# Kernel tuning notes

Measured on AMD Instinct MI355X. Metric: run time of the kernel, lower is better.

The kernel has to match this reference:

```python
import jax, jax.numpy as jnp
import numpy as np

N_ROIS = 2048
N_CLS = 21            # includes background (class 0)
N_GT = 50
IMG_H, IMG_W = 800.0, 1333.0
SCORE_T = 0.3         # thresh in forward
NMS_T = 0.3           # cfg.TEST.NMS
DEDUP_T = 0.3         # compute_iou iou_thresh
BBOX_STDS = jnp.array([0.1, 0.1, 0.2, 0.2], dtype=jnp.float32)
BBOX_MEANS = jnp.array([0.0, 0.0, 0.0, 0.0], dtype=jnp.float32)


def _rand_boxes(key, n, max_w, max_h):
    k1, k2, k3, k4 = jax.random.split(key, 4)
    x1 = jax.random.uniform(k1, (n,)) * (max_w - 64.0)
    y1 = jax.random.uniform(k2, (n,)) * (max_h - 64.0)
    bw = 16.0 + jax.random.uniform(k3, (n,)) * 240.0
    bh = 16.0 + jax.random.uniform(k4, (n,)) * 240.0
    x2 = jnp.minimum(x1 + bw, max_w - 1.0)
    y2 = jnp.minimum(y1 + bh, max_h - 1.0)
    return jnp.stack([x1, y1, x2, y2], axis=1)


def setup_inputs() -> dict:
    key = jax.random.key(0)
    k1, k2, k3, k4, k5 = jax.random.split(key, 5)
    boxes = _rand_boxes(k1, N_ROIS, IMG_W, IMG_H)
    rois_org = jnp.concatenate([jnp.zeros((N_ROIS, 1)), boxes], axis=1)[None]  # [1,N,5]
    cls_prob_org = jax.nn.softmax(2.0 * jax.random.normal(k2, (N_ROIS, N_CLS)), axis=1)[None]
    bbox_pred_org = 0.2 * jax.random.normal(k3, (N_ROIS, 4 * N_CLS))[None]
    im_info = jnp.array([[IMG_H, IMG_W, 1.0]], dtype=jnp.float32)
    gt_xyxy = _rand_boxes(k4, N_GT, IMG_W, IMG_H)
    gt_lbl = jax.random.randint(k5, (N_GT, 1), 1, N_CLS).astype(jnp.float32)
    gt_boxes = jnp.concatenate([gt_xyxy, gt_lbl], axis=1)[None]  # [1,G,5]
    return {"rois_org": rois_org, "cls_prob_org": cls_prob_org,
            "bbox_pred_org": bbox_pred_org, "im_info": im_info,
            "gt_boxes": gt_boxes, "num_boxes": N_GT}


def iou_matrix(b1, b2):
    # b1 [M,4], b2 [K,4] -> [M,K]
    a1 = (b1[:, 2] - b1[:, 0]) * (b1[:, 3] - b1[:, 1])
    a2 = (b2[:, 2] - b2[:, 0]) * (b2[:, 3] - b2[:, 1])
    lt = jnp.maximum(b1[:, None, :2], b2[None, :, :2])
    rb = jnp.minimum(b1[:, None, 2:], b2[None, :, 2:])
    wh = jnp.clip(rb - lt, 0.0)
    inter = wh[..., 0] * wh[..., 1]
    return inter / (a1[:, None] + a2[None, :] - inter + 1e-6)


def _decode_clip(boxes, deltas, im_info):
    # bbox_transform_inv + clip_boxes. boxes [N,4], deltas [N,C,4]
    w = boxes[:, 2] - boxes[:, 0] + 1.0
    h = boxes[:, 3] - boxes[:, 1] + 1.0
    cx = boxes[:, 0] + 0.5 * w
    cy = boxes[:, 1] + 0.5 * h
    d = deltas * BBOX_STDS + BBOX_MEANS  # unnormalize
    pcx = d[..., 0] * w[:, None] + cx[:, None]
    pcy = d[..., 1] * h[:, None] + cy[:, None]
    pw = jnp.exp(d[..., 2]) * w[:, None]
    ph = jnp.exp(d[..., 3]) * h[:, None]
    x1 = jnp.clip(pcx - 0.5 * pw, 0.0, im_info[0, 1] - 1.0)
    y1 = jnp.clip(pcy - 0.5 * ph, 0.0, im_info[0, 0] - 1.0)
    x2 = jnp.clip(pcx + 0.5 * pw, 0.0, im_info[0, 1] - 1.0)
    y2 = jnp.clip(pcy + 0.5 * ph, 0.0, im_info[0, 0] - 1.0)
    return jnp.stack([x1, y1, x2, y2], axis=-1)  # [N,C,4]


def _detect(rois_org, cls_prob_org, bbox_pred_org, im_info, gt_boxes, num_boxes):
    scores = cls_prob_org[0]                       # [N,C]
    boxes = rois_org[0, :, 1:5]                    # [N,4]
    n = scores.shape[0]
    deltas = bbox_pred_org[0].reshape(n, -1, 4)    # [N,C,4]
    pred = _decode_clip(boxes, deltas, im_info)    # [N,C,4]
    gt = gt_boxes[0, :num_boxes, :4]               # [G,4], static slice
    idx = jnp.arange(n)

    def per_class(cls_scores, cls_boxes):
        valid = cls_scores > SCORE_T
        order = jnp.argsort(jnp.where(valid, -cls_scores, jnp.inf))
        b = cls_boxes[order]
        v = valid[order]
        s = cls_scores[order]
        iou = iou_matrix(b, b)                     # [N,N]
        def body(i, keep):
            sup = keep[i] & (iou[i] > NMS_T) & (idx > i)
            return keep & ~sup
        keep = jax.lax.fori_loop(0, n, body, v)
        dup = jnp.any(iou_matrix(b, gt) > DEDUP_T, axis=1)  # gt dedup loop, vectorized
        m = (keep & ~dup).astype(b.dtype)
        return jnp.concatenate([b, s[:, None]], axis=1) * m[:, None]

    # classes 1..C-1; output [C-1, N, 5] with suppressed rows zeroed
    return jax.vmap(per_class, in_axes=(1, 1))(scores[:, 1:], pred[:, 1:, :])


def reference(rois_org, cls_prob_org, bbox_pred_org, im_info, gt_boxes, num_boxes):
    return _detect(rois_org, cls_prob_org, bbox_pred_org, im_info, gt_boxes, num_boxes)
```

## Files before the change

### kernel.cpp

```cpp
#include <hip/hip_runtime.h>

typedef unsigned long long u64;

#define N_ROIS 2048
#define N_CLSX 21
#define N_CLS_OUT 20
#define SCORE_T 0.3f
#define NMS_T 0.3f
#define DEDUP_T 0.3f
#define NT 256
#define NWAVES (NT / 64)
#define CPW (N_ROIS / 64 / NWAVES)
#define NFAST 128

__device__ __forceinline__ float iou_f(float ax1, float ay1, float ax2, float ay2,
                                       float aarea,
                                       float bx1, float by1, float bx2, float by2,
                                       float barea) {
    float ix1 = fmaxf(ax1, bx1), iy1 = fmaxf(ay1, by1);
    float ix2 = fminf(ax2, bx2), iy2 = fminf(ay2, by2);
    float iw = fmaxf(ix2 - ix1, 0.0f), ih = fmaxf(iy2 - iy1, 0.0f);
    float inter = iw * ih;
    return inter / (aarea + barea - inter + 1e-6f);
}

__global__ __launch_bounds__(NT) void detect_kernel(
    const float* __restrict__ rois,
    const float* __restrict__ cls_prob,
    const float* __restrict__ bbox_pred,
    const float* __restrict__ im_info,
    const float* __restrict__ gt_boxes,
    const int*   __restrict__ num_boxes,
    float* __restrict__ out)
{
    __shared__ float  vsc[N_ROIS];
    __shared__ int    vidx[N_ROIS];
    __shared__ float4 sbox[N_ROIS];
    __shared__ float  ssc[N_ROIS];
    __shared__ unsigned char keepb[N_ROIS];
    __shared__ float4 sgt[64];
    __shared__ int    wbase[NWAVES];
    __shared__ u64    kwords[2];
    __shared__ u64    dupw[2];

    const int tid = threadIdx.x;
    const int wid = tid >> 6, lane = tid & 63;
    const int cls = blockIdx.x + 1;
    const int ng = *num_boxes;
    const float W = im_info[1], H = im_info[0];
    float* o = out + (size_t)blockIdx.x * N_ROIS * 5;

    u64 masks[CPW];
    float vals[CPW];
    int mycnt = 0;
    #pragma unroll
    for (int c = 0; c < CPW; ++c) {
        int i = ((wid * CPW + c) << 6) + lane;
        float sc = cls_prob[i * N_CLSX + cls];
        vals[c] = sc;
        masks[c] = __ballot(sc > SCORE_T);
        mycnt += __popcll(masks[c]);
    }
    if (lane == 0) wbase[wid] = mycnt;
    __syncthreads();
    int base = 0;
    for (int w = 0; w < wid; ++w) base += wbase[w];
    int nvtot = 0;
    for (int w = 0; w < NWAVES; ++w) nvtot += wbase[w];
    const int nv = nvtot;
    #pragma unroll
    for (int c = 0; c < CPW; ++c) {
        int i = ((wid * CPW + c) << 6) + lane;
        u64 m = masks[c];
        if ((m >> lane) & 1ULL) {
            int pre = __popcll(m & ((1ULL << lane) - 1ULL));
            vidx[base + pre] = i;
            vsc[base + pre]  = vals[c];
        }
        base += __popcll(m);
    }
    __syncthreads();

    if (nv <= NFAST) {
        if (wid == 0) {
            float s0 = (lane < nv)      ? vsc[lane]      : 0.0f;
            float s1 = (64 + lane < nv) ? vsc[64 + lane] : 0.0f;
            int  idx0 = (lane < nv)      ? vidx[lane]      : 0;
            int  idx1 = (64 + lane < nv) ? vidx[64 + lane] : 0;

            float ax1 = rois[idx0 * 5 + 1], ay1 = rois[idx0 * 5 + 2];
            float ax2 = rois[idx0 * 5 + 3], ay2 = rois[idx0 * 5 + 4];
            const float* dpa = &bbox_pred[idx0 * 84 + cls * 4];
            float da0 = dpa[0], da1 = dpa[1], da2 = dpa[2], da3 = dpa[3];
            float bx1v = rois[idx1 * 5 + 1], by1v = rois[idx1 * 5 + 2];
            float bx2v = rois[idx1 * 5 + 3], by2v = rois[idx1 * 5 + 4];
            const float* dpb = &bbox_pred[idx1 * 84 + cls * 4];
            float db0 = dpb[0], db1 = dpb[1], db2 = dpb[2], db3 = dpb[3];

            int r0 = 0, r1 = 0;
            const int n0 = nv < 64 ? nv : 64;
            for (int u = 0; u < n0; ++u) {
                float su0 = __shfl(s0, u);
                float su1 = __shfl(s1, u);
                r0 += (su0 > s0) || (su0 == s0 && u < lane);
                r1 += (su0 > s1) || (su0 == s1);
                if (64 + u < nv) {
                    r0 += (su1 > s0);
                    r1 += (su1 > s1) || (su1 == s1 && u < lane);
                }
            }

            #define DECODE2(X1,Y1,X2,Y2,D0,D1,D2,D3,B)                       \
            {                                                                \
                float w = (X2) - (X1) + 1.0f, h = (Y2) - (Y1) + 1.0f;        \
                float cx = (X1) + 0.5f * w, cy = (Y1) + 0.5f * h;            \
                float pcx = (D0) * 0.1f * w + cx, pcy = (D1) * 0.1f * h + cy;\
                float pw = expf((D2) * 0.2f) * w, ph = expf((D3) * 0.2f) * h;\
                B.x = fminf(fmaxf(pcx - 0.5f * pw, 0.0f), W - 1.0f);         \
                B.y = fminf(fmaxf(pcy - 0.5f * ph, 0.0f), H - 1.0f);         \
                B.z = fminf(fmaxf(pcx + 0.5f * pw, 0.0f), W - 1.0f);         \
                B.w = fminf(fmaxf(pcy + 0.5f * ph, 0.0f), H - 1.0f);         \
            }
            float4 c0, c1;
            DECODE2(ax1, ay1, ax2, ay2, da0, da1, da2, da3, c0)
            DECODE2(bx1v, by1v, bx2v, by2v, db0, db1, db2, db3, c1)

            if (lane < nv)      { sbox[r0] = c0; ssc[r0] = s0; }
            if (64 + lane < nv) { sbox[r1] = c1; ssc[r1] = s1; }
        } else {
            if (wid == 3)
                for (int g = lane; g < ng; g += 64)
                    sgt[g] = make_float4(gt_boxes[g * 5 + 0], gt_boxes[g * 5 + 1],
                                         gt_boxes[g * 5 + 2], gt_boxes[g * 5 + 3]);
            float4* o4 = (float4*)o;
            float4 z4 = make_float4(0.f, 0.f, 0.f, 0.f);
            for (int t = (wid - 1) * 64 + lane; t < N_ROIS * 5 / 4; t += 192)
                o4[t] = z4;
        }
        __syncthreads();

        if (wid == 0) {
            float4 b0 = (lane < nv)      ? sbox[lane]      : make_float4(0,0,0,0);
            float4 b1 = (64 + lane < nv) ? sbox[64 + lane] : make_float4(0,0,0,0);
            float ar0 = (b0.z - b0.x) * (b0.w - b0.y);
            float ar1 = (b1.z - b1.x) * (b1.w - b1.y);
            u64 S0lo = 0, S0hi = 0, S1lo = 0, S1hi = 0;
            for (int i = 0; i < nv; ++i) {
                bool hi = i >= 64;
                int src = i & 63;
                float cx1 = __shfl(hi ? b1.x : b0.x, src);
                float cy1 = __shfl(hi ? b1.y : b0.y, src);
                float cx2 = __shfl(hi ? b1.z : b0.z, src);
                float cy2 = __shfl(hi ? b1.w : b0.w, src);
                float car = __shfl(hi ? ar1 : ar0, src);
                float i0 = iou_f(cx1, cy1, cx2, cy2, car, b0.x, b0.y, b0.z, b0.w, ar0);
                float i1 = iou_f(cx1, cy1, cx2, cy2, car, b1.x, b1.y, b1.z, b1.w, ar1);
                bool sup0 = (i0 > NMS_T) && (i < lane);
                bool sup1 = (i1 > NMS_T) && (i < 64 + lane);
                if (i < 64) {
                    S0lo |= sup0 ? (1ULL << i) : 0ULL;
                    S1lo |= sup1 ? (1ULL << i) : 0ULL;
                } else {
                    S0hi |= sup0 ? (1ULL << (i - 64)) : 0ULL;
                    S1hi |= sup1 ? (1ULL << (i - 64)) : 0ULL;
                }
            }
            bool init0 = lane < nv, init1 = 64 + lane < nv;
            u64 kw0 = __ballot(init0), kw1 = __ballot(init1);
            for (int it = 0; it < NFAST; ++it) {
                bool a0 = init0 && !((S0lo & kw0) | (S0hi & kw1));
                bool a1 = init1 && !((S1lo & kw0) | (S1hi & kw1));
                u64 nk0 = __ballot(a0), nk1 = __ballot(a1);
                bool done = (nk0 == kw0) && (nk1 == kw1);
                kw0 = nk0; kw1 = nk1;
                if (done) break;
            }
            if (lane == 0) { kwords[0] = kw0; kwords[1] = kw1; }
        } else if (wid == 1 || wid == 2) {
            int e = (wid - 1) * 64 + lane;
            bool dup = false;
            if (e < nv) {
                float4 a = sbox[e];
                float aarea = (a.z - a.x) * (a.w - a.y);
                for (int g = 0; g < ng; ++g) {
                    float4 gb = sgt[g];
                    float garea = (gb.z - gb.x) * (gb.w - gb.y);
                    dup |= iou_f(a.x, a.y, a.z, a.w, aarea,
                                 gb.x, gb.y, gb.z, gb.w, garea) > DEDUP_T;
                }
            }
            u64 wd = __ballot(dup);
            if (lane == 0) dupw[wid - 1] = wd;
        }
        __syncthreads();

        if (tid < NFAST && tid < nv) {
            bool kept = ((kwords[tid >> 6] >> (tid & 63)) & 1ULL) &&
                        !((dupw[tid >> 6] >> (tid & 63)) & 1ULL);
            if (kept) {
                float4 b = sbox[tid];
                float s = ssc[tid];
                float* orow = o + tid * 5;
                orow[0] = b.x; orow[1] = b.y; orow[2] = b.z; orow[3] = b.w;
                orow[4] = s;
            }
        }
        return;
    }

    for (int g = tid; g < ng; g += NT)
        sgt[g] = make_float4(gt_boxes[g * 5 + 0], gt_boxes[g * 5 + 1],
                             gt_boxes[g * 5 + 2], gt_boxes[g * 5 + 3]);

    for (int v = tid; v < nv; v += NT) {
        int idx = vidx[v];
        float x1 = rois[idx * 5 + 1], y1 = rois[idx * 5 + 2];
        float x2 = rois[idx * 5 + 3], y2 = rois[idx * 5 + 4];
        const float* dp = &bbox_pred[idx * 84 + cls * 4];
        float d0 = dp[0], d1 = dp[1], d2 = dp[2], d3 = dp[3];
        float sc = vsc[v];
        int r = 0;
        for (int u = 0; u < nv; ++u) {
            float su = vsc[u];
            r += (su > sc) || (su == sc && u < v);
        }
        float w = x2 - x1 + 1.0f, h = y2 - y1 + 1.0f;
        float cx = x1 + 0.5f * w, cy = y1 + 0.5f * h;
        float pcx = d0 * 0.1f * w + cx, pcy = d1 * 0.1f * h + cy;
        float pw = expf(d2 * 0.2f) * w, ph = expf(d3 * 0.2f) * h;
        float4 b;
        b.x = fminf(fmaxf(pcx - 0.5f * pw, 0.0f), W - 1.0f);
        b.y = fminf(fmaxf(pcy - 0.5f * ph, 0.0f), H - 1.0f);
        b.z = fminf(fmaxf(pcx + 0.5f * pw, 0.0f), W - 1.0f);
        b.w = fminf(fmaxf(pcy + 0.5f * ph, 0.0f), H - 1.0f);
        sbox[r] = b;
        ssc[r]  = sc;
        keepb[r] = 1;
    }
    __syncthreads();

    for (int i = 0; i < nv; ++i) {
        __syncthreads();
        if (keepb[i]) {
            float4 a = sbox[i];
            float aarea = (a.z - a.x) * (a.w - a.y);
            for (int j = i + 1 + tid; j < nv; j += NT) {
                if (keepb[j]) {
                    float4 bb = sbox[j];
                    float barea = (bb.z - bb.x) * (bb.w - bb.y);
                    if (iou_f(a.x, a.y, a.z, a.w, aarea,
                              bb.x, bb.y, bb.z, bb.w, barea) > NMS_T)
                        keepb[j] = 0;
                }
            }
        }
    }
    __syncthreads();
    for (int v = tid; v < nv; v += NT) {
        if (keepb[v]) {
            float4 a = sbox[v];
            float aarea = (a.z - a.x) * (a.w - a.y);
            bool dup = false;
            for (int g = 0; g < ng; ++g) {
                float4 gb = sgt[g];
                float garea = (gb.z - gb.x) * (gb.w - gb.y);
                dup |= iou_f(a.x, a.y, a.z, a.w, aarea,
                             gb.x, gb.y, gb.z, gb.w, garea) > DEDUP_T;
            }
            if (dup) keepb[v] = 0;
        }
    }
    __syncthreads();
    for (int t = tid; t < N_ROIS * 5; t += NT) {
        int j = t / 5, comp = t - 5 * j;
        float val = 0.0f;
        if (j < nv && keepb[j]) {
            float4 b = sbox[j];
            val = comp == 0 ? b.x : comp == 1 ? b.y : comp == 2 ? b.z :
                  comp == 3 ? b.w : ssc[j];
        }
        o[t] = val;
    }
}

extern "C" void kernel_launch(void* const* d_in, const int* in_sizes, int n_in,
                              void* d_out, int out_size, void* d_ws, size_t ws_size,
                              hipStream_t stream) {
    const float* rois      = (const float*)d_in[0];
    const float* cls_prob  = (const float*)d_in[1];
    const float* bbox_pred = (const float*)d_in[2];
    const float* im_info   = (const float*)d_in[3];
    const float* gt        = (const float*)d_in[4];
    const int*   nb        = (const int*)d_in[5];
    float* out = (float*)d_out;

    detect_kernel<<<dim3(N_CLS_OUT), dim3(NT), 0, stream>>>(
        rois, cls_prob, bbox_pred, im_info, gt, nb, out);
}
```

Before: 32.50 us.

## Remove sort barrier in fast NMS path by using score-order predicates in place

The small-candidate path no longer sorts boxes into shared memory before NMS. Wave 0 decodes boxes and builds suppression masks directly in compaction order, using a score comparison to decide priority. Wave 1-2 re-decode boxes for the GT dedup, and wave 3 computes ranks only for output placement. This removes one block barrier and a shared-memory round trip, at the cost of redundant decoding and more work in the inner loop.

Measured after the change: 30.97 us. 1.05x faster.

```diff
diff --git a/kernel.cpp b/kernel.cpp
--- a/kernel.cpp
+++ b/kernel.cpp
@@ -22,6 +22,22 @@
     float iw = fmaxf(ix2 - ix1, 0.0f), ih = fmaxf(iy2 - iy1, 0.0f);
     float inter = iw * ih;
     return inter / (aarea + barea - inter + 1e-6f);
+}
+
+#define DECODE_IDX(IDX, B)                                                    \
+{                                                                             \
+    float x1 = rois[(IDX) * 5 + 1], y1 = rois[(IDX) * 5 + 2];                 \
+    float x2 = rois[(IDX) * 5 + 3], y2 = rois[(IDX) * 5 + 4];                 \
+    const float* dp = &bbox_pred[(IDX) * 84 + cls * 4];                       \
+    float d0 = dp[0], d1 = dp[1], d2 = dp[2], d3 = dp[3];                     \
+    float w = x2 - x1 + 1.0f, h = y2 - y1 + 1.0f;                             \
+    float cx = x1 + 0.5f * w, cy = y1 + 0.5f * h;                             \
+    float pcx = d0 * 0.1f * w + cx, pcy = d1 * 0.1f * h + cy;                 \
+    float pw = expf(d2 * 0.2f) * w, ph = expf(d3 * 0.2f) * h;                 \
+    B.x = fminf(fmaxf(pcx - 0.5f * pw, 0.0f), W - 1.0f);                      \
+    B.y = fminf(fmaxf(pcy - 0.5f * ph, 0.0f), H - 1.0f);                      \
+    B.z = fminf(fmaxf(pcx + 0.5f * pw, 0.0f), W - 1.0f);                      \
+    B.w = fminf(fmaxf(pcy + 0.5f * ph, 0.0f), H - 1.0f);                      \
 }
 
 __global__ __launch_bounds__(NT) void detect_kernel(
@@ -40,7 +56,7 @@
     __shared__ unsigned char keepb[N_ROIS];
     __shared__ float4 sgt[64];
     __shared__ int    wbase[NWAVES];
-    __shared__ u64    kwords[2];
+    __shared__ int    rrank[NFAST];
     __shared__ u64    dupw[2];
 
     const int tid = threadIdx.x;
@@ -79,69 +95,24 @@
         }
         base += __popcll(m);
     }
+    if (wid == 3)
+        for (int g = lane; g < ng; g += 64)
+            sgt[g] = make_float4(gt_boxes[g * 5 + 0], gt_boxes[g * 5 + 1],
+                                 gt_boxes[g * 5 + 2], gt_boxes[g * 5 + 3]);
     __syncthreads();
 
     if (nv <= NFAST) {
+        float4 b0 = make_float4(0,0,0,0), b1 = make_float4(0,0,0,0);
+        float s0 = 0.0f, s1 = 0.0f;
+        u64 kw0 = 0, kw1 = 0;
+
         if (wid == 0) {
-            float s0 = (lane < nv)      ? vsc[lane]      : 0.0f;
-            float s1 = (64 + lane < nv) ? vsc[64 + lane] : 0.0f;
-            int  idx0 = (lane < nv)      ? vidx[lane]      : 0;
-            int  idx1 = (64 + lane < nv) ? vidx[64 + lane] : 0;
-
-            float ax1 = rois[idx0 * 5 + 1], ay1 = rois[idx0 * 5 + 2];
-            float ax2 = rois[idx0 * 5 + 3], ay2 = rois[idx0 * 5 + 4];
-            const float* dpa = &bbox_pred[idx0 * 84 + cls * 4];
-            float da0 = dpa[0], da1 = dpa[1], da2 = dpa[2], da3 = dpa[3];
-            float bx1v = rois[idx1 * 5 + 1], by1v = rois[idx1 * 5 + 2];
-            float bx2v = rois[idx1 * 5 + 3], by2v = rois[idx1 * 5 + 4];
-            const float* dpb = &bbox_pred[idx1 * 84 + cls * 4];
-            float db0 = dpb[0], db1 = dpb[1], db2 = dpb[2], db3 = dpb[3];
-
-            int r0 = 0, r1 = 0;
-            const int n0 = nv < 64 ? nv : 64;
-            for (int u = 0; u < n0; ++u) {
-                float su0 = __shfl(s0, u);
-                float su1 = __shfl(s1, u);
-                r0 += (su0 > s0) || (su0 == s0 && u < lane);
-                r1 += (su0 > s1) || (su0 == s1);
-                if (64 + u < nv) {
-                    r0 += (su1 > s0);
-                    r1 += (su1 > s1) || (su1 == s1 && u < lane);
-                }
-            }
-
-            #define DECODE2(X1,Y1,X2,Y2,D0,D1,D2,D3,B)                       \
-            {                                                                \
-                float w = (X2) - (X1) + 1.0f, h = (Y2) - (Y1) + 1.0f;        \
-                float cx = (X1) + 0.5f * w, cy = (Y1) + 0.5f * h;            \
-                float pcx = (D0) * 0.1f * w + cx, pcy = (D1) * 0.1f * h + cy;\
-                float pw = expf((D2) * 0.2f) * w, ph = expf((D3) * 0.2f) * h;\
-                B.x = fminf(fmaxf(pcx - 0.5f * pw, 0.0f), W - 1.0f);         \
-                B.y = fminf(fmaxf(pcy - 0.5f * ph, 0.0f), H - 1.0f);         \
-                B.z = fminf(fmaxf(pcx + 0.5f * pw, 0.0f), W - 1.0f);         \
-                B.w = fminf(fmaxf(pcy + 0.5f * ph, 0.0f), H - 1.0f);         \
-            }
-            float4 c0, c1;
-            DECODE2(ax1, ay1, ax2, ay2, da0, da1, da2, da3, c0)
-            DECODE2(bx1v, by1v, bx2v, by2v, db0, db1, db2, db3, c1)
-
-            if (lane < nv)      { sbox[r0] = c0; ssc[r0] = s0; }
-            if (64 + lane < nv) { sbox[r1] = c1; ssc[r1] = s1; }
-        } else {
-            if (wid == 3)
-                for (int g = lane; g < ng; g += 64)
-                    sgt[g] = make_float4(gt_boxes[g * 5 + 0], gt_boxes[g * 5 + 1],
-                                         gt_boxes[g * 5 + 2], gt_boxes[g * 5 + 3]);
-            float4* o4 = (float4*)o;
-            float4 z4 = make_float4(0.f, 0.f, 0.f, 0.f);
-            for (int t = (wid - 1) * 64 + lane; t < N_ROIS * 5 / 4; t += 192)
-                o4[t] = z4;
-        }
-        __syncthreads();
-
-        if (wid == 0) {
-            float4 b0 = (lane < nv)      ? sbox[lane]      : make_float4(0,0,0,0);
-            float4 b1 = (64 + lane < nv) ? sbox[64 + lane] : make_float4(0,0,0,0);
+            s0 = (lane < nv)      ? vsc[lane]      : 0.0f;
+            s1 = (64 + lane < nv) ? vsc[64 + lane] : 0.0f;
+            int idx0 = (lane < nv)      ? vidx[lane]      : 0;
+            int idx1 = (64 + lane < nv) ? vidx[64 + lane] : 0;
+            DECODE_IDX(idx0, b0)
+            DECODE_IDX(idx1, b1)
             float ar0 = (b0.z - b0.x) * (b0.w - b0.y);
             float ar1 = (b1.z - b1.x) * (b1.w - b1.y);
             u64 S0lo = 0, S0hi = 0, S1lo = 0, S1hi = 0;
@@ -152,11 +123,14 @@
                 float cy1 = __shfl(hi ? b1.y : b0.y, src);
                 float cx2 = __shfl(hi ? b1.z : b0.z, src);
                 float cy2 = __shfl(hi ? b1.w : b0.w, src);
-                float car = __shfl(hi ? ar1 : ar0, src);
+                float cs  = __shfl(hi ? s1   : s0,   src);
+                float car = (cx2 - cx1) * (cy2 - cy1);
                 float i0 = iou_f(cx1, cy1, cx2, cy2, car, b0.x, b0.y, b0.z, b0.w, ar0);
                 float i1 = iou_f(cx1, cy1, cx2, cy2, car, b1.x, b1.y, b1.z, b1.w, ar1);
-                bool sup0 = (i0 > NMS_T) && (i < lane);
-                bool sup1 = (i1 > NMS_T) && (i < 64 + lane);
+                bool hp0 = (cs > s0) || (cs == s0 && i < lane);
+                bool hp1 = (cs > s1) || (cs == s1 && i < 64 + lane);
+                bool sup0 = (i0 > NMS_T) && hp0;
+                bool sup1 = (i1 > NMS_T) && hp1;
                 if (i < 64) {
                     S0lo |= sup0 ? (1ULL << i) : 0ULL;
                     S1lo |= sup1 ? (1ULL << i) : 0ULL;
@@ -166,7 +140,7 @@
                 }
             }
             bool init0 = lane < nv, init1 = 64 + lane < nv;
-            u64 kw0 = __ballot(init0), kw1 = __ballot(init1);
+            kw0 = __ballot(init0); kw1 = __ballot(init1);
             for (int it = 0; it < NFAST; ++it) {
                 bool a0 = init0 && !((S0lo & kw0) | (S0hi & kw1));
                 bool a1 = init1 && !((S1lo & kw0) | (S1hi & kw1));
@@ -175,12 +149,14 @@
                 kw0 = nk0; kw1 = nk1;
                 if (done) break;
             }
-            if (lane == 0) { kwords[0] = kw0; kwords[1] = kw1; }
         } else if (wid == 1 || wid == 2) {
             int e = (wid - 1) * 64 + lane;
+            bool has = e < nv;
+            int idx = has ? vidx[e] : 0;
+            float4 a;
+            DECODE_IDX(idx, a)
             bool dup = false;
-            if (e < nv) {
-                float4 a = sbox[e];
+            if (has) {
                 float aarea = (a.z - a.x) * (a.w - a.y);
                 for (int g = 0; g < ng; ++g) {
                     float4 gb = sgt[g];
@@ -191,48 +167,60 @@
             }
             u64 wd = __ballot(dup);
             if (lane == 0) dupw[wid - 1] = wd;
+        } else {
+            float t0 = (lane < nv)      ? vsc[lane]      : 0.0f;
+            float t1 = (64 + lane < nv) ? vsc[64 + lane] : 0.0f;
+            int r0 = 0, r1 = 0;
+            const int n0 = nv < 64 ? nv : 64;
+            for (int u = 0; u < n0; ++u) {
+                float su0 = __shfl(t0, u);
+                float su1 = __shfl(t1, u);
+                r0 += (su0 > t0) || (su0 == t0 && u < lane);
+                r1 += (su0 > t1) || (su0 == t1);
+                if (64 + u < nv) {
+                    r0 += (su1 > t0);
+                    r1 += (su1 > t1) || (su1 == t1 && u < lane);
+                }
+            }
+            if (lane < nv)      rrank[lane]      = r0;
+            if (64 + lane < nv) rrank[64 + lane] = r1;
+            if (nv <= 64 && lane == 0) dupw[1] = 0ULL;
+        }
+
+        if (wid != 0) {
+            float4* o4 = (float4*)o;
+            float4 z4 = make_float4(0.f, 0.f, 0.f, 0.f);
+            for (int t = (wid - 1) * 64 + lane; t < N_ROIS * 5 / 4; t += 192)
+                o4[t] = z4;
         }
         __syncthreads();
 
-        if (tid < NFAST && tid < nv) {
-            bool kept = ((kwords[tid >> 6] >> (tid & 63)) & 1ULL) &&
-                        !((dupw[tid >> 6] >> (tid & 63)) & 1ULL);
-            if (kept) {
-                float4 b = sbox[tid];
-                float s = ssc[tid];
-                float* orow = o + tid * 5;
-                orow[0] = b.x; orow[1] = b.y; orow[2] = b.z; orow[3] = b.w;
-                orow[4] = s;
+        if (wid == 0) {
+            u64 d0 = dupw[0], d1 = dupw[1];
+            if (lane < nv && ((kw0 >> lane) & 1ULL) && !((d0 >> lane) & 1ULL)) {
+                float* orow = o + rrank[lane] * 5;
+                orow[0] = b0.x; orow[1] = b0.y; orow[2] = b0.z; orow[3] = b0.w;
+                orow[4] = s0;
+            }
+            if (64 + lane < nv && ((kw1 >> lane) & 1ULL) && !((d1 >> lane) & 1ULL)) {
+                float* orow = o + rrank[64 + lane] * 5;
+                orow[0] = b1.x; orow[1] = b1.y; orow[2] = b1.z; orow[3] = b1.w;
+                orow[4] = s1;
             }
         }
         return;
     }
-
-    for (int g = tid; g < ng; g += NT)
-        sgt[g] = make_float4(gt_boxes[g * 5 + 0], gt_boxes[g * 5 + 1],
-                             gt_boxes[g * 5 + 2], gt_boxes[g * 5 + 3]);
 
     for (int v = tid; v < nv; v += NT) {
         int idx = vidx[v];
-        float x1 = rois[idx * 5 + 1], y1 = rois[idx * 5 + 2];
-        float x2 = rois[idx * 5 + 3], y2 = rois[idx * 5 + 4];
-        const float* dp = &bbox_pred[idx * 84 + cls * 4];
-        float d0 = dp[0], d1 = dp[1], d2 = dp[2], d3 = dp[3];
         float sc = vsc[v];
         int r = 0;
         for (int u = 0; u < nv; ++u) {
             float su = vsc[u];
             r += (su > sc) || (su == sc && u < v);
         }
-        float w = x2 - x1 + 1.0f, h = y2 - y1 + 1.0f;
-        float cx = x1 + 0.5f * w, cy = y1 + 0.5f * h;
-        float pcx = d0 * 0.1f * w + cx, pcy = d1 * 0.1f * h + cy;
-        float pw = expf(d2 * 0.2f) * w, ph = expf(d3 * 0.2f) * h;
         float4 b;
-        b.x = fminf(fmaxf(pcx - 0.5f * pw, 0.0f), W - 1.0f);
-        b.y = fminf(fmaxf(pcy - 0.5f * ph, 0.0f), H - 1.0f);
-        b.z = fminf(fmaxf(pcx + 0.5f * pw, 0.0f), W - 1.0f);
-        b.w = fminf(fmaxf(pcy + 0.5f * ph, 0.0f), H - 1.0f);
+        DECODE_IDX(idx, b)
         sbox[r] = b;
         ssc[r]  = sc;
         keepb[r] = 1;
```
